# Kernel optimization log

Hardware: AMD Instinct MI355X
Metric: run time of the kernel (lower is better)

The kernel has to match this reference:

```python
import jax, jax.numpy as jnp
import numpy as np

NEG_SLOPE_GAT = 0.2   # GATConv internal leaky_relu slope (PyG default)
NEG_SLOPE = 0.01      # nn.LeakyReLU default slope


def _gat(h_src_in, h_dst_in, src, dst, Wsrc, Wdst, a_s, a_d, b, n_dst, self_loops):
    """Single-head PyG-style GATConv: gather -> score -> edge softmax -> scatter-sum."""
    hs = h_src_in @ Wsrc            # [N_src, C]
    hd = h_dst_in @ Wdst            # [N_dst, C]
    if self_loops:                  # static flag; same node set on both sides
        loop = jnp.arange(n_dst, dtype=src.dtype)
        src = jnp.concatenate([src, loop])
        dst = jnp.concatenate([dst, loop])
    # attention logits per edge
    e = jax.nn.leaky_relu((hs @ a_s)[src] + (hd @ a_d)[dst], NEG_SLOPE_GAT)  # [E]
    # softmax over edges sharing a destination node
    m = jax.ops.segment_max(e, dst, num_segments=n_dst)
    ex = jnp.exp(e - m[dst])
    denom = jax.ops.segment_sum(ex, dst, num_segments=n_dst)
    alpha = ex / denom[dst]
    out = jax.ops.segment_sum(hs[src] * alpha[:, None], dst, num_segments=n_dst)
    return out + b


def setup_inputs() -> dict:
    key = jax.random.key(0)
    ks = iter(jax.random.split(key, 64))
    NB, NP = 100_000, 50_000
    E_bb, E_pp, E_bp = 800_000, 400_000, 400_000
    FB, FP, H, H2 = 32, 34, 64, 32
    rn = lambda shape, s=0.05: jax.random.normal(next(ks), shape, jnp.float32) * s
    d = {}
    d['x_b'] = rn((NB, FB), 1.0)
    d['x_p'] = rn((NP, FP), 1.0)
    d['ei_bb'] = jax.random.randint(next(ks), (2, E_bb), 0, NB, jnp.int32)
    d['ei_pp'] = jax.random.randint(next(ks), (2, E_pp), 0, NP, jnp.int32)
    d['ei_bp_src'] = jax.random.randint(next(ks), (E_bp,), 0, NB, jnp.int32)
    d['ei_bp_dst'] = jax.random.randint(next(ks), (E_bp,), 0, NP, jnp.int32)
    d['W_in_b'] = rn((FB, H)); d['b_in_b'] = jnp.zeros((H,), jnp.float32)
    d['W_in_p'] = rn((FP, H)); d['b_in_p'] = jnp.zeros((H,), jnp.float32)
    for tag, cin, cout in (('1', H, H), ('2', H, H2)):
        d['W_bb' + tag] = rn((cin, cout)); d['as_bb' + tag] = rn((cout,)); d['ad_bb' + tag] = rn((cout,)); d['b_bb' + tag] = jnp.zeros((cout,), jnp.float32)
        d['W_pp' + tag] = rn((cin, cout)); d['as_pp' + tag] = rn((cout,)); d['ad_pp' + tag] = rn((cout,)); d['b_pp' + tag] = jnp.zeros((cout,), jnp.float32)
        d['Ws_bp' + tag] = rn((cin, cout)); d['Wd_bp' + tag] = rn((cin, cout)); d['as_bp' + tag] = rn((cout,)); d['ad_bp' + tag] = rn((cout,)); d['b_bp' + tag] = jnp.zeros((cout,), jnp.float32)
    d['W_out'] = rn((H2, 1)); d['b_out'] = jnp.zeros((1,), jnp.float32)
    return d


def reference(x_b, x_p, ei_bb, ei_pp, ei_bp_src, ei_bp_dst,
              W_in_b, b_in_b, W_in_p, b_in_p,
              W_bb1, as_bb1, ad_bb1, b_bb1, W_pp1, as_pp1, ad_pp1, b_pp1,
              Ws_bp1, Wd_bp1, as_bp1, ad_bp1, b_bp1,
              W_bb2, as_bb2, ad_bb2, b_bb2, W_pp2, as_pp2, ad_pp2, b_pp2,
              Ws_bp2, Wd_bp2, as_bp2, ad_bp2, b_bp2,
              W_out, b_out):
    NB, NP = x_b.shape[0], x_p.shape[0]
    lr = lambda v: jax.nn.leaky_relu(v, NEG_SLOPE)
    # input projections (dropout is eval-mode identity)
    hb = lr(x_b @ W_in_b + b_in_b)
    hp = lr(x_p @ W_in_p + b_in_p)
    # hetero conv 1 (sum aggregation over relations sharing a dst type)
    ob = _gat(hb, hb, ei_bb[0], ei_bb[1], W_bb1, W_bb1, as_bb1, ad_bb1, b_bb1, NB, True)
    op = (_gat(hp, hp, ei_pp[0], ei_pp[1], W_pp1, W_pp1, as_pp1, ad_pp1, b_pp1, NP, True)
          + _gat(hb, hp, ei_bp_src, ei_bp_dst, Ws_bp1, Wd_bp1, as_bp1, ad_bp1, b_bp1, NP, False))
    hb, hp = lr(ob), lr(op)
    # hetero conv 2
    ob2 = _gat(hb, hb, ei_bb[0], ei_bb[1], W_bb2, W_bb2, as_bb2, ad_bb2, b_bb2, NB, True)
    op2 = (_gat(hp, hp, ei_pp[0], ei_pp[1], W_pp2, W_pp2, as_pp2, ad_pp2, b_pp2, NP, True)
           + _gat(hb, hp, ei_bp_src, ei_bp_dst, Ws_bp2, Wd_bp2, as_bp2, ad_bp2, b_bp2, NP, False))
    hp = lr(op2)
    return hp @ W_out + b_out  # [NP, 1]
```

## Files before the change

### kernel.cpp

```cpp
#include <hip/hip_runtime.h>
#include <hip/hip_bf16.h>
#include <cstdint>
#include <cstddef>


typedef __attribute__((ext_vector_type(8))) short short8;
typedef __attribute__((ext_vector_type(4))) float f32x4;
typedef unsigned int u32;
typedef __hip_bfloat16 bf16;

#define ABITS 9
#define CHUNKE 8192

static __device__ __forceinline__ float b2f(bf16 v) { return __bfloat162float(v); }

static __device__ __forceinline__ float ldf(const void* p, int i, int bf) {
    return bf ? __bfloat162float(((const bf16*)p)[i]) : ((const float*)p)[i];
}

static __device__ __forceinline__ short f2bs(float f) {
    bf16 h = __float2bfloat16(f);
    return *reinterpret_cast<short*>(&h);
}
static __device__ __forceinline__ float bs2f(short s) {
    bf16 h = *reinterpret_cast<bf16*>(&s);
    return __bfloat162float(h);
}
static __device__ __forceinline__ float lo16(u32 u) { return bs2f((short)(u & 0xffffu)); }
static __device__ __forceinline__ float hi16(u32 u) { return bs2f((short)(u >> 16)); }
static __device__ __forceinline__ u32 pack2(float x, float y) {
    return (u32)(unsigned short)f2bs(x) | ((u32)(unsigned short)f2bs(y) << 16);
}
static __device__ __forceinline__ float sel4(const float* a, int i) {
    return i == 0 ? a[0] : i == 1 ? a[1] : i == 2 ? a[2] : a[3];
}
static __device__ __forceinline__ float lrelu2(float x) { return x > 0.f ? x : 0.2f * x; }

static __device__ __forceinline__ int probe_bf(const unsigned* __restrict__ w, int* cnt) {
    if (threadIdx.x == 0) *cnt = 0;
    __syncthreads();
    int c = 0;
#pragma unroll
    for (int j = 0; j < 4; ++j) {
        unsigned u = w[threadIdx.x * 4 + j];
        unsigned e = (u >> 7) & 0xffu;
        c += (e >= 100u && e <= 145u) ? 1 : 0;
    }
    atomicAdd(cnt, c);
    __syncthreads();
    int r = (*cnt > 614) ? 1 : 0;
    __syncthreads();
    return r;
}

template <int CIN>
static __device__ __forceinline__ void in_proj_body(
    short* WT, float* bl, int bid,
    const void* __restrict__ X, const void* __restrict__ W, const void* __restrict__ B,
    bf16* __restrict__ Y, int M, int bf)
{
    constexpr int KP = 40;
    for (int i = threadIdx.x; i < 64 * CIN; i += 256) {
        int n = i / CIN, k = i - n * CIN;
        WT[n * KP + k] = f2bs(ldf(W, k * 64 + n, bf));
    }
    if (threadIdx.x < 64) bl[threadIdx.x] = ldf(B, threadIdx.x, bf);
    __syncthreads();

    int lane = threadIdx.x & 63;
    int wv   = threadIdx.x >> 6;
    int m = lane & 15, quad = lane >> 4;
    int row0 = (bid * 4 + wv) * 16;
    if (row0 >= M) return;

    int arow = row0 + m; if (arow >= M) arow = M - 1;
    short8 a;
#pragma unroll
    for (int j = 0; j < 8; ++j)
        a[j] = f2bs(ldf(X, arow * CIN + quad * 8 + j, bf));

    f32x4 acc[4] = {};
#pragma unroll
    for (int tt = 0; tt < 4; ++tt) {
        short8 bfr = *(const short8*)&WT[((lane & 15) + 16 * tt) * KP + quad * 8];
        acc[tt] = __builtin_amdgcn_mfma_f32_16x16x32_bf16(a, bfr, acc[tt], 0, 0, 0);
    }

    if (CIN == 34) {
        float x32[4], x33[4];
#pragma unroll
        for (int r = 0; r < 4; ++r) {
            int row = row0 + quad * 4 + r; if (row >= M) row = M - 1;
            x32[r] = ldf(X, row * CIN + 32, bf);
            x33[r] = ldf(X, row * CIN + 33, bf);
        }
#pragma unroll
        for (int tt = 0; tt < 4; ++tt) {
            int col = (lane & 15) + 16 * tt;
            float w32 = bs2f(WT[col * KP + 32]);
            float w33 = bs2f(WT[col * KP + 33]);
#pragma unroll
            for (int r = 0; r < 4; ++r)
                acc[tt][r] += x32[r] * w32 + x33[r] * w33;
        }
    }

#pragma unroll
    for (int tt = 0; tt < 4; ++tt) {
        int col = (lane & 15) + 16 * tt;
        float bb = bl[col];
#pragma unroll
        for (int r = 0; r < 4; ++r) {
            int row = row0 + quad * 4 + r;
            if (row < M) {
                float v = acc[tt][r] + bb;
                v = v > 0.f ? v : 0.01f * v;
                Y[(size_t)row * 64 + col] = __float2bfloat16(v);
            }
        }
    }
}

__global__ __launch_bounds__(256) void k_hist_inproj(
    const int* __restrict__ bb_d, const int* __restrict__ pp_d,
    const int* __restrict__ bp_d, int* __restrict__ histM,
    const unsigned* __restrict__ probe_w, int* __restrict__ flag,
    int E_bb, int E_pp, int E_bp, int NB, int NP, int nbkt, int nblk,
    const void* __restrict__ Xb, const void* __restrict__ Wb, const void* __restrict__ Bb,
    bf16* __restrict__ Yb, int MB,
    const void* __restrict__ Xp, const void* __restrict__ Wp, const void* __restrict__ Bp,
    bf16* __restrict__ Yp, int MP)
{
    __shared__ short WT[64 * 40];
    __shared__ float bl[64];
    __shared__ int aux[1 << ABITS];
    if ((int)blockIdx.x < nblk) {
        if (blockIdx.x == 0) {
            int b = probe_bf(probe_w, &aux[0]);
            if (threadIdx.x == 0) *flag = b;
        }
        for (int i = threadIdx.x; i < nbkt; i += 256) aux[i] = 0;
        __syncthreads();
        int E_all = E_bb + E_pp + E_bp;
        int base = blockIdx.x * CHUNKE;
        int end = base + CHUNKE < E_all ? base + CHUNKE : E_all;
        for (int i = base + threadIdx.x; i < end; i += 256) {
            int d;
            if (i < E_bb) d = bb_d[i];
            else if (i < E_bb + E_pp) d = NB + pp_d[i - E_bb];
            else d = NB + NP + bp_d[i - E_bb - E_pp];
            atomicAdd(&aux[d >> ABITS], 1);
        }
        __syncthreads();
        for (int i = threadIdx.x; i < nbkt; i += 256)
            histM[(size_t)i * nblk + blockIdx.x] = aux[i];
    } else {
        int bfv = probe_bf(probe_w, &aux[0]);
        int bid = blockIdx.x - nblk;
        int nbb = (MB + 63) >> 6;
        if (bid < nbb) in_proj_body<32>(WT, bl, bid, Xb, Wb, Bb, Yb, MB, bfv);
        else           in_proj_body<34>(WT, bl, bid - nbb, Xp, Wp, Bp, Yp, MP, bfv);
    }
}

__global__ __launch_bounds__(1024) void k_scan1(const int* __restrict__ deg,
                                                int* __restrict__ out,
                                                int* __restrict__ bsum, int n)
{
    __shared__ int wsum[16];
    int gid = blockIdx.x * 1024 + threadIdx.x;
    int lane = threadIdx.x & 63, wid = threadIdx.x >> 6;
    int v = (gid < n) ? deg[gid] : 0;
    int x = v;
#pragma unroll
    for (int off = 1; off < 64; off <<= 1) {
        int y = __shfl_up(x, off, 64);
        if (lane >= off) x += y;
    }
    if (lane == 63) wsum[wid] = x;
    __syncthreads();
    if (wid == 0 && lane < 16) {
        int w0 = wsum[lane];
#pragma unroll
        for (int off = 1; off < 16; off <<= 1) {
            int y = __shfl_up(w0, off, 16);
            if (lane >= off) w0 += y;
        }
        wsum[lane] = w0;
    }
    __syncthreads();
    int base = (wid > 0) ? wsum[wid - 1] : 0;
    int incl = base + x;
    if (gid < n) out[gid] = incl - v;
    if (threadIdx.x == 1023) bsum[blockIdx.x] = incl;
}

__global__ __launch_bounds__(1024) void k_scan2(int* __restrict__ bsum, int nb)
{
    __shared__ int wsum[16];
    int lane = threadIdx.x & 63, wid = threadIdx.x >> 6;
    int v = (threadIdx.x < nb) ? bsum[threadIdx.x] : 0;
    int x = v;
#pragma unroll
    for (int off = 1; off < 64; off <<= 1) {
        int y = __shfl_up(x, off, 64);
        if (lane >= off) x += y;
    }
    if (lane == 63) wsum[wid] = x;
    __syncthreads();
    if (wid == 0 && lane < 16) {
        int w0 = wsum[lane];
#pragma unroll
        for (int off = 1; off < 16; off <<= 1) {
            int y = __shfl_up(w0, off, 16);
            if (lane >= off) w0 += y;
        }
        wsum[lane] = w0;
    }
    __syncthreads();
    int base = (wid > 0) ? wsum[wid - 1] : 0;
    if (threadIdx.x < nb) bsum[threadIdx.x] = base + x - v;
}

__global__ __launch_bounds__(1024) void k_scan3(int* __restrict__ indptr,
                                                const int* __restrict__ bsum,
                                                int n, int E)
{
    int gid = blockIdx.x * 1024 + threadIdx.x;
    if (gid < n) indptr[gid] += bsum[blockIdx.x];
    if (gid == 0) indptr[n] = E;
}

template <int N1, int N2, bool S1F, bool S2F>
static __device__ __forceinline__ void dual_body(
    short* WT, int bid, const bf16* __restrict__ H,
    const void* __restrict__ W1, const void* __restrict__ W2,
    const void* __restrict__ as1, const void* __restrict__ ad1,
    const void* __restrict__ as2, const void* __restrict__ ad2,
    bf16* __restrict__ HS1, bf16* __restrict__ HS2,
    float* __restrict__ SS1, float* __restrict__ SD1,
    float* __restrict__ SS2, float* __restrict__ SD2,
    int M, int bf)
{
    constexpr int KP = 72;
    constexpr int T1 = N1 / 16, T2 = N2 / 16, T = T1 + T2;
    for (int i = threadIdx.x; i < N1 * 64; i += 256) {
        int n = i >> 6, k = i & 63;
        WT[n * KP + k] = f2bs(ldf(W1, k * N1 + n, bf));
    }
    for (int i = threadIdx.x; i < N2 * 64; i += 256) {
        int n = i >> 6, k = i & 63;
        WT[(N1 + n) * KP + k] = f2bs(ldf(W2, k * N2 + n, bf));
    }
    __syncthreads();

    int lane = threadIdx.x & 63;
    int wv   = threadIdx.x >> 6;
    int m = lane & 15, quad = lane >> 4;
    int row0 = (bid * 4 + wv) * 16;
    if (row0 >= M) return;

    const short* Hs = (const short*)H;
    int arow = row0 + m; if (arow >= M) arow = M - 1;

    f32x4 acc[T] = {};
#pragma unroll
    for (int ks = 0; ks < 2; ++ks) {
        short8 a = *(const short8*)&Hs[(size_t)arow * 64 + ks * 32 + quad * 8];
#pragma unroll
        for (int tt = 0; tt < T; ++tt) {
            short8 bfr = *(const short8*)&WT[((lane & 15) + 16 * tt) * KP + ks * 32 + quad * 8];
            acc[tt] = __builtin_amdgcn_mfma_f32_16x16x32_bf16(a, bfr, acc[tt], 0, 0, 0);
        }
    }

    float vs1[4] = {}, vd1[4] = {}, vs2[4] = {}, vd2[4] = {};
#pragma unroll
    for (int tt = 0; tt < T1; ++tt) {
        int col = (lane & 15) + 16 * tt;
        float av = ldf(as1, col, bf), dv = ldf(ad1, col, bf);
#pragma unroll
        for (int r = 0; r < 4; ++r) {
            vs1[r] += acc[tt][r] * av;
            vd1[r] += acc[tt][r] * dv;
        }
    }
#pragma unroll
    for (int tt = 0; tt < T2; ++tt) {
        int col = (lane & 15) + 16 * tt;
        float av = ldf(as2, col, bf), dv = ldf(ad2, col, bf);
#pragma unroll
        for (int r = 0; r < 4; ++r) {
            vs2[r] += acc[T1 + tt][r] * av;
            vd2[r] += acc[T1 + tt][r] * dv;
        }
    }
#pragma unroll
    for (int off = 1; off < 16; off <<= 1)
#pragma unroll
        for (int r = 0; r < 4; ++r) {
            vs1[r] += __shfl_xor(vs1[r], off);
            vd1[r] += __shfl_xor(vd1[r], off);
            vs2[r] += __shfl_xor(vs2[r], off);
            vd2[r] += __shfl_xor(vd2[r], off);
        }
    int c = lane & 15;
    {
        int row = row0 + quad * 4 + (c & 3);
        if (row < M) {
            if (c < 4)       SS1[row] = sel4(vs1, c & 3);
            else if (c < 8)  SD1[row] = sel4(vd1, c & 3);
            else if (c < 12) SS2[row] = sel4(vs2, c & 3);
            else             SD2[row] = sel4(vd2, c & 3);
        }
    }

    if (S1F) {
#pragma unroll
        for (int tt = 0; tt < T1; ++tt) {
            int col = (lane & 15) + 16 * tt;
#pragma unroll
            for (int r = 0; r < 4; ++r) {
                int row = row0 + quad * 4 + r;
                if (row < M)
                    HS1[(size_t)row * N1 + col] = __float2bfloat16(acc[tt][r]);
            }
        }
    }
    if (S2F) {
#pragma unroll
        for (int tt = 0; tt < T2; ++tt) {
            int col = (lane & 15) + 16 * tt;
#pragma unroll
            for (int r = 0; r < 4; ++r) {
                int row = row0 + quad * 4 + r;
                if (row < M)
                    HS2[(size_t)row * N2 + col] = __float2bfloat16(acc[T1 + tt][r]);
            }
        }
    }
}

template <int N, bool STORE>
static __device__ __forceinline__ void proj_body(
    short* WT, int bid, const bf16* __restrict__ H, const void* __restrict__ W,
    const void* __restrict__ a_s, const void* __restrict__ a_d,
    bf16* __restrict__ HS, float* __restrict__ SS, float* __restrict__ SD,
    int M, int bf)
{
    constexpr int KP = 72;
    constexpr int T = N / 16;
    for (int i = threadIdx.x; i < N * 64; i += 256) {
        int n = i >> 6, k = i & 63;
        WT[n * KP + k] = f2bs(ldf(W, k * N + n, bf));
    }
    __syncthreads();

    int lane = threadIdx.x & 63;
    int wv   = threadIdx.x >> 6;
    int m = lane & 15, quad = lane >> 4;
    int row0 = (bid * 4 + wv) * 16;
    if (row0 >= M) return;

    const short* Hs = (const short*)H;
    int arow = row0 + m; if (arow >= M) arow = M - 1;

    f32x4 acc[T] = {};
#pragma unroll
    for (int ks = 0; ks < 2; ++ks) {
        short8 a = *(const short8*)&Hs[(size_t)arow * 64 + ks * 32 + quad * 8];
#pragma unroll
        for (int tt = 0; tt < T; ++tt) {
            short8 bfr = *(const short8*)&WT[((lane & 15) + 16 * tt) * KP + ks * 32 + quad * 8];
            acc[tt] = __builtin_amdgcn_mfma_f32_16x16x32_bf16(a, bfr, acc[tt], 0, 0, 0);
        }
    }

    float asv[T], adv[T];
#pragma unroll
    for (int tt = 0; tt < T; ++tt) {
        int col = (lane & 15) + 16 * tt;
        asv[tt] = ldf(a_s, col, bf);
        adv[tt] = ldf(a_d, col, bf);
    }
    float vs[4] = {}, vd[4] = {};
#pragma unroll
    for (int tt = 0; tt < T; ++tt)
#pragma unroll
        for (int r = 0; r < 4; ++r) {
            vs[r] += acc[tt][r] * asv[tt];
            vd[r] += acc[tt][r] * adv[tt];
        }
#pragma unroll
    for (int off = 1; off < 16; off <<= 1)
#pragma unroll
        for (int r = 0; r < 4; ++r) {
            vs[r] += __shfl_xor(vs[r], off);
            vd[r] += __shfl_xor(vd[r], off);
        }
    int c = lane & 15;
    if (c < 8) {
        int row = row0 + quad * 4 + (c & 3);
        if (row < M) {
            if (c < 4) SS[row] = sel4(vs, c & 3);
            else       SD[row] = sel4(vd, c & 3);
        }
    }

    if (STORE) {
#pragma unroll
        for (int tt = 0; tt < T; ++tt) {
            int col = (lane & 15) + 16 * tt;
#pragma unroll
            for (int r = 0; r < 4; ++r) {
                int row = row0 + quad * 4 + r;
                if (row < M)
                    HS[(size_t)row * N + col] = __float2bfloat16(acc[tt][r]);
            }
        }
    }
}

__global__ __launch_bounds__(256) void k_scatter_dual(
    const int* __restrict__ bb_s, const int* __restrict__ bb_d,
    const int* __restrict__ pp_s, const int* __restrict__ pp_d,
    const int* __restrict__ bp_s, const int* __restrict__ bp_d,
    const int* __restrict__ histS, unsigned* __restrict__ ebuf,
    int E_bb, int E_pp, int E_bp, int NB, int NP, int nbkt, int nblk,
    const bf16* __restrict__ hb,
    const void* W_bb1, const void* Ws_bp1,
    const void* as_bb1, const void* ad_bb1, const void* as_bp1, const void* ad_bp1,
    bf16* hs_bb, bf16* hs_bp,
    float* ss_bb, float* sd_bb, float* ss_bp, float* junkNB, int MB,
    const bf16* __restrict__ hp,
    const void* W_pp1, const void* Wd_bp1,
    const void* as_pp1, const void* ad_pp1,
    bf16* hs_pp, float* ss_pp, float* sd_pp, float* junkNP, float* sd_bp, int MP,
    const int* __restrict__ flag)
{
    __shared__ short WT[128 * 72];
    if ((int)blockIdx.x < nblk) {
        int* cur = (int*)WT;
        for (int i = threadIdx.x; i < nbkt; i += 256)
            cur[i] = histS[(size_t)i * nblk + blockIdx.x];
        __syncthreads();
        int E_all = E_bb + E_pp + E_bp;
        int base = blockIdx.x * CHUNKE;
        int end = base + CHUNKE < E_all ? base + CHUNKE : E_all;
        for (int i = base + threadIdx.x; i < end; i += 256) {
            int s, d;
            if (i < E_bb) { s = bb_s[i]; d = bb_d[i]; }
            else if (i < E_bb + E_pp) { int j = i - E_bb; s = pp_s[j]; d = NB + pp_d[j]; }
            else { int j = i - E_bb - E_pp; s = bp_s[j]; d = NB + NP + bp_d[j]; }
            int p = atomicAdd(&cur[d >> ABITS], 1);
            ebuf[p] = ((unsigned)(d & ((1 << ABITS) - 1)) << 20) | (unsigned)s;
        }
    } else {
        const int bfv = *flag;
        int bid = blockIdx.x - nblk;
        int nbb = (MB + 63) >> 6;
        if (bid < nbb)
            dual_body<64, 64, true, true>(WT, bid, hb, W_bb1, Ws_bp1,
                as_bb1, ad_bb1, as_bp1, ad_bp1, hs_bb, hs_bp,
                ss_bb, sd_bb, ss_bp, junkNB, MB, bfv);
        else
            dual_body<64, 64, true, false>(WT, bid - nbb, hp, W_pp1, Wd_bp1,
                as_pp1, ad_pp1, as_bp1, ad_bp1, hs_pp, nullptr,
                ss_pp, sd_pp, junkNP, sd_bp, MP, bfv);
    }
}

__global__ __launch_bounds__(256) void k_finalize(
    const unsigned* __restrict__ ebuf, const int* __restrict__ histS,
    int* __restrict__ ip_all, int2* __restrict__ sw,
    const float* __restrict__ ss_bb, const float* __restrict__ sd_bb,
    const float* __restrict__ ss_pp, const float* __restrict__ sd_pp,
    const float* __restrict__ ss_bp, const float* __restrict__ sd_bp,
    int NB, int NP, int NALL, int E_all, int nbkt, int nblk)
{
    __shared__ int h[1 << ABITS];
    __shared__ int pre[1 << ABITS];
    __shared__ int wq[4];
    int b = blockIdx.x;
    int d0 = b << ABITS;
    int nloc = NALL - d0 < (1 << ABITS) ? NALL - d0 : (1 << ABITS);
    int t = threadIdx.x;
    for (int i = t; i < (1 << ABITS); i += 256) h[i] = 0;
    __syncthreads();
    int s0 = histS[(size_t)b * nblk];
    int s1 = histS[(size_t)(b + 1) * nblk];
    for (int i = s0 + t; i < s1; i += 256)
        atomicAdd(&h[ebuf[i] >> 20], 1);
    __syncthreads();
    int v0 = h[2 * t], v1 = h[2 * t + 1];
    int ps = v0 + v1;
    int lane = t & 63, wid = t >> 6;
    int x = ps;
#pragma unroll
    for (int off = 1; off < 64; off <<= 1) {
        int y = __shfl_up(x, off, 64);
        if (lane >= off) x += y;
    }
    if (lane == 63) wq[wid] = x;
    __syncthreads();
    if (t == 0) {
        int a = 0;
#pragma unroll
        for (int w = 0; w < 4; ++w) { int tmp = wq[w]; wq[w] = a; a += tmp; }
    }
    __syncthreads();
    int excl = wq[wid] + x - ps;
    pre[2 * t]     = excl;
    pre[2 * t + 1] = excl + v0;
    __syncthreads();
    for (int i = t; i < nloc; i += 256) ip_all[d0 + i] = s0 + pre[i];
    if (d0 + nloc == NALL && t == 0) ip_all[NALL] = E_all;
    for (int i = t; i < (1 << ABITS); i += 256) h[i] = s0 + pre[i];
    __syncthreads();
    for (int i = s0 + t; i < s1; i += 256) {
        unsigned e = ebuf[i];
        int dl = (int)(e >> 20);
        int src = (int)(e & 0xFFFFFu);
        int p = atomicAdd(&h[dl], 1);
        int d = d0 + dl;
        float ssv, sdv;
        if (d < NB)           { ssv = ss_bb[src]; sdv = sd_bb[d]; }
        else if (d < NB + NP) { ssv = ss_pp[src]; sdv = sd_pp[d - NB]; }
        else                  { ssv = ss_bp[src]; sdv = sd_bp[d - NB - NP]; }
        int2 pk; pk.x = src; pk.y = __float_as_int(__expf(lrelu2(ssv + sdv)));
        sw[p] = pk;
    }
}

static __device__ __forceinline__ void gather1_body(
    int bid, const int* __restrict__ ip, const int2* __restrict__ sw,
    const float* __restrict__ SS, const float* __restrict__ SD,
    const bf16* __restrict__ HS, const void* __restrict__ bias,
    bf16* __restrict__ OUT, int M, int bf)
{
    int lane = threadIdx.x & 63;
    int half = lane >> 5, hl = lane & 31;
    int d = bid * 4 + (threadIdx.x >> 6);
    if (d >= M) return;
    const u32* H32 = (const u32*)HS;
    float ax = 0.f, ay = 0.f, den = 0.f;
    if (half == 0) {
        float ex = __expf(lrelu2(SS[d] + SD[d]));
        u32 h = H32[(size_t)d * 32 + hl];
        ax = lo16(h) * ex; ay = hi16(h) * ex; den = ex;
    }
    int j1 = ip[d + 1];
    int j = ip[d] + half;
    for (; j + 6 < j1; j += 8) {
        int2 p0 = sw[j], p1 = sw[j + 2], p2 = sw[j + 4], p3 = sw[j + 6];
        u32 h0 = H32[(size_t)p0.x * 32 + hl];
        u32 h1 = H32[(size_t)p1.x * 32 + hl];
        u32 h2 = H32[(size_t)p2.x * 32 + hl];
        u32 h3 = H32[(size_t)p3.x * 32 + hl];
        float e0 = __int_as_float(p0.y), e1 = __int_as_float(p1.y);
        float e2 = __int_as_float(p2.y), e3 = __int_as_float(p3.y);
        ax += lo16(h0) * e0 + lo16(h1) * e1 + lo16(h2) * e2 + lo16(h3) * e3;
        ay += hi16(h0) * e0 + hi16(h1) * e1 + hi16(h2) * e2 + hi16(h3) * e3;
        den += (e0 + e1) + (e2 + e3);
    }
    for (; j < j1; j += 2) {
        int2 p0 = sw[j];
        u32 h0 = H32[(size_t)p0.x * 32 + hl];
        float e0 = __int_as_float(p0.y);
        ax += lo16(h0) * e0; ay += hi16(h0) * e0; den += e0;
    }
    ax += __shfl_xor(ax, 32); ay += __shfl_xor(ay, 32); den += __shfl_xor(den, 32);
    if (half == 0) {
        float vx = ax / den + ldf(bias, 2 * hl, bf);
        float vy = ay / den + ldf(bias, 2 * hl + 1, bf);
        vx = vx > 0.f ? vx : 0.01f * vx;
        vy = vy > 0.f ? vy : 0.01f * vy;
        ((u32*)OUT)[(size_t)d * 32 + hl] = pack2(vx, vy);
    }
}

static __device__ __forceinline__ void gather2_body(
    int bid, const int* __restrict__ ip1, const int2* __restrict__ sw,
    const float* __restrict__ SS1, const float* __restrict__ SD1,
    const bf16* __restrict__ HS1,
    const int* __restrict__ ip2, const bf16* __restrict__ HS2,
    const void* __restrict__ b1, const void* __restrict__ b2,
    bf16* __restrict__ OUT, int M, int bf)
{
    int lane = threadIdx.x & 63;
    int half = lane >> 5, hl = lane & 31;
    int d = bid * 4 + (threadIdx.x >> 6);
    if (d >= M) return;
    const u32* H1 = (const u32*)HS1;
    const u32* H2 = (const u32*)HS2;
    float a1x = 0.f, a1y = 0.f, den1 = 0.f;
    if (half == 0) {
        float ex = __expf(lrelu2(SS1[d] + SD1[d]));
        u32 h = H1[(size_t)d * 32 + hl];
        a1x = lo16(h) * ex; a1y = hi16(h) * ex; den1 = ex;
    }
    int j1 = ip1[d + 1];
    int j = ip1[d] + half;
    for (; j + 6 < j1; j += 8) {
        int2 p0 = sw[j], p1 = sw[j + 2], p2 = sw[j + 4], p3 = sw[j + 6];
        u32 h0 = H1[(size_t)p0.x * 32 + hl];
        u32 h1 = H1[(size_t)p1.x * 32 + hl];
        u32 h2 = H1[(size_t)p2.x * 32 + hl];
        u32 h3 = H1[(size_t)p3.x * 32 + hl];
        float e0 = __int_as_float(p0.y), e1 = __int_as_float(p1.y);
        float e2 = __int_as_float(p2.y), e3 = __int_as_float(p3.y);
        a1x += lo16(h0) * e0 + lo16(h1) * e1 + lo16(h2) * e2 + lo16(h3) * e3;
        a1y += hi16(h0) * e0 + hi16(h1) * e1 + hi16(h2) * e2 + hi16(h3) * e3;
        den1 += (e0 + e1) + (e2 + e3);
    }
    for (; j < j1; j += 2) {
        int2 p0 = sw[j];
        u32 h0 = H1[(size_t)p0.x * 32 + hl];
        float e0 = __int_as_float(p0.y);
        a1x += lo16(h0) * e0; a1y += hi16(h0) * e0; den1 += e0;
    }
    float a2x = 0.f, a2y = 0.f, den2 = 0.f;
    j1 = ip2[d + 1];
    j = ip2[d] + half;
    for (; j + 6 < j1; j += 8) {
        int2 p0 = sw[j], p1 = sw[j + 2], p2 = sw[j + 4], p3 = sw[j + 6];
        u32 h0 = H2[(size_t)p0.x * 32 + hl];
        u32 h1 = H2[(size_t)p1.x * 32 + hl];
        u32 h2 = H2[(size_t)p2.x * 32 + hl];
        u32 h3 = H2[(size_t)p3.x * 32 + hl];
        float e0 = __int_as_float(p0.y), e1 = __int_as_float(p1.y);
        float e2 = __int_as_float(p2.y), e3 = __int_as_float(p3.y);
        a2x += lo16(h0) * e0 + lo16(h1) * e1 + lo16(h2) * e2 + lo16(h3) * e3;
        a2y += hi16(h0) * e0 + hi16(h1) * e1 + hi16(h2) * e2 + hi16(h3) * e3;
        den2 += (e0 + e1) + (e2 + e3);
    }
    for (; j < j1; j += 2) {
        int2 p0 = sw[j];
        u32 h0 = H2[(size_t)p0.x * 32 + hl];
        float e0 = __int_as_float(p0.y);
        a2x += lo16(h0) * e0; a2y += hi16(h0) * e0; den2 += e0;
    }
    a1x += __shfl_xor(a1x, 32); a1y += __shfl_xor(a1y, 32); den1 += __shfl_xor(den1, 32);
    a2x += __shfl_xor(a2x, 32); a2y += __shfl_xor(a2y, 32); den2 += __shfl_xor(den2, 32);
    if (half == 0) {
        float inv2 = den2 > 0.f ? 1.f / den2 : 0.f;
        float vx = a1x / den1 + a2x * inv2 + ldf(b1, 2 * hl, bf) + ldf(b2, 2 * hl, bf);
        float vy = a1y / den1 + a2y * inv2 + ldf(b1, 2 * hl + 1, bf) + ldf(b2, 2 * hl + 1, bf);
        vx = vx > 0.f ? vx : 0.01f * vx;
        vy = vy > 0.f ? vy : 0.01f * vy;
        ((u32*)OUT)[(size_t)d * 32 + hl] = pack2(vx, vy);
    }
}

__global__ __launch_bounds__(256) void k_gather12(
    const int* __restrict__ ip_bb, const int2* __restrict__ sw,
    const float* __restrict__ ss_bb, const float* __restrict__ sd_bb,
    const bf16* __restrict__ hs_bb, const void* __restrict__ b_bb1,
    bf16* __restrict__ hb2, int NB,
    const int* __restrict__ ip_pp, const int* __restrict__ ip_bp,
    const float* __restrict__ ss_pp, const float* __restrict__ sd_pp,
    const bf16* __restrict__ hs_pp, const bf16* __restrict__ hs_bp,
    const void* __restrict__ b_pp1, const void* __restrict__ b_bp1,
    bf16* __restrict__ hp2, int NP,
    const int* __restrict__ flag)
{
    const int bf = *flag;
    int nbb = (NB + 3) >> 2;
    if ((int)blockIdx.x < nbb)
        gather1_body(blockIdx.x, ip_bb, sw, ss_bb, sd_bb, hs_bb, b_bb1, hb2, NB, bf);
    else
        gather2_body(blockIdx.x - nbb, ip_pp, sw, ss_pp, sd_pp, hs_pp,
                     ip_bp, hs_bp, b_pp1, b_bp1, hp2, NP, bf);
}

__global__ __launch_bounds__(256) void k_proj2_all(
    const bf16* __restrict__ hp2,
    const void* W_pp2, const void* Wd_bp2,
    const void* as_pp2, const void* ad_pp2, const void* as_bp2, const void* ad_bp2,
    bf16* hs2_pp, float* ss2_pp, float* sd2_pp, float* junkNP, float* sd2_bp, int MP,
    const bf16* __restrict__ hb2,
    const void* Ws_bp2, bf16* hs2_bp, float* ss2_bp, float* junkNB, int MB,
    const int* __restrict__ flag)
{
    const int bf = *flag;
    __shared__ short WT[64 * 72];
    int npb = (MP + 63) >> 6;
    if ((int)blockIdx.x < npb)
        dual_body<32, 32, true, false>(WT, blockIdx.x, hp2, W_pp2, Wd_bp2,
            as_pp2, ad_pp2, as_bp2, ad_bp2, hs2_pp, nullptr,
            ss2_pp, sd2_pp, junkNP, sd2_bp, MP, bf);
    else
        proj_body<32, true>(WT, blockIdx.x - npb, hb2, Ws_bp2,
            as_bp2, ad_bp2, hs2_bp, ss2_bp, junkNB, MB, bf);
}

__global__ __launch_bounds__(256) void k_gather_out(
    const int* __restrict__ ip1, const int2* __restrict__ sw,
    const float* __restrict__ SS1, const float* __restrict__ SD1,
    const bf16* __restrict__ HS1,
    const int* __restrict__ ip2,
    const float* __restrict__ SS2, const float* __restrict__ SD2,
    const bf16* __restrict__ HS2,
    const void* __restrict__ b1, const void* __restrict__ b2,
    const void* __restrict__ Wout, const void* __restrict__ bout,
    void* __restrict__ OUT, int M, const int* __restrict__ flag)
{
    const int bf = *flag;
    int lane = threadIdx.x & 63;
    int q = lane >> 4, hl = lane & 15;
    int d = blockIdx.x * 4 + (threadIdx.x >> 6);
    if (d >= M) return;
    const u32* H1 = (const u32*)HS1;
    const u32* H2 = (const u32*)HS2;
    float sdd = SD1[d];
    float a1x = 0.f, a1y = 0.f, den1 = 0.f;
    if (q == 0) {
        float ex = __expf(lrelu2(SS1[d] + sdd));
        u32 h = H1[(size_t)d * 16 + hl];
        a1x = lo16(h) * ex; a1y = hi16(h) * ex; den1 = ex;
    }
    int j1 = ip1[d + 1];
    int j = ip1[d] + q;
    for (; j + 4 < j1; j += 8) {
        int s0 = sw[j].x, s1 = sw[j + 4].x;
        u32 h0 = H1[(size_t)s0 * 16 + hl];
        u32 h1 = H1[(size_t)s1 * 16 + hl];
        float e0 = __expf(lrelu2(SS1[s0] + sdd));
        float e1 = __expf(lrelu2(SS1[s1] + sdd));
        a1x += lo16(h0) * e0 + lo16(h1) * e1;
        a1y += hi16(h0) * e0 + hi16(h1) * e1;
        den1 += e0 + e1;
    }
    if (j < j1) {
        int s0 = sw[j].x;
        u32 h0 = H1[(size_t)s0 * 16 + hl];
        float e0 = __expf(lrelu2(SS1[s0] + sdd));
        a1x += lo16(h0) * e0; a1y += hi16(h0) * e0; den1 += e0;
    }
    float sdd2 = SD2[d];
    float a2x = 0.f, a2y = 0.f, den2 = 0.f;
    j1 = ip2[d + 1];
    j = ip2[d] + q;
    for (; j + 4 < j1; j += 8) {
        int s0 = sw[j].x, s1 = sw[j + 4].x;
        u32 h0 = H2[(size_t)s0 * 16 + hl];
        u32 h1 = H2[(size_t)s1 * 16 + hl];
        float e0 = __expf(lrelu2(SS2[s0] + sdd2));
        float e1 = __expf(lrelu2(SS2[s1] + sdd2));
        a2x += lo16(h0) * e0 + lo16(h1) * e1;
        a2y += hi16(h0) * e0 + hi16(h1) * e1;
        den2 += e0 + e1;
    }
    if (j < j1) {
        int s0 = sw[j].x;
        u32 h0 = H2[(size_t)s0 * 16 + hl];
        float e0 = __expf(lrelu2(SS2[s0] + sdd2));
        a2x += lo16(h0) * e0; a2y += hi16(h0) * e0; den2 += e0;
    }
    a1x += __shfl_xor(a1x, 16); a1y += __shfl_xor(a1y, 16); den1 += __shfl_xor(den1, 16);
    a2x += __shfl_xor(a2x, 16); a2y += __shfl_xor(a2y, 16); den2 += __shfl_xor(den2, 16);
    a1x += __shfl_xor(a1x, 32); a1y += __shfl_xor(a1y, 32); den1 += __shfl_xor(den1, 32);
    a2x += __shfl_xor(a2x, 32); a2y += __shfl_xor(a2y, 32); den2 += __shfl_xor(den2, 32);
    float inv2 = den2 > 0.f ? 1.f / den2 : 0.f;
    float vx = a1x / den1 + a2x * inv2 + ldf(b1, 2 * hl, bf) + ldf(b2, 2 * hl, bf);
    float vy = a1y / den1 + a2y * inv2 + ldf(b1, 2 * hl + 1, bf) + ldf(b2, 2 * hl + 1, bf);
    vx = vx > 0.f ? vx : 0.01f * vx;
    vy = vy > 0.f ? vy : 0.01f * vy;
    float t = vx * ldf(Wout, 2 * hl, bf) + vy * ldf(Wout, 2 * hl + 1, bf);
#pragma unroll
    for (int off = 1; off < 16; off <<= 1) t += __shfl_xor(t, off);
    if (lane == 0) {
        float r = t + ldf(bout, 0, bf);
        if (bf) ((bf16*)OUT)[d] = __float2bfloat16(r);
        else    ((float*)OUT)[d] = r;
    }
}

extern "C" void kernel_launch(void* const* d_in, const int* in_sizes, int n_in,
                              void* d_out, int out_size, void* d_ws, size_t ws_size,
                              hipStream_t stream)
{
    const void* x_b = d_in[0];
    const void* x_p = d_in[1];
    const int* ei_bb = (const int*)d_in[2];
    const int* ei_pp = (const int*)d_in[3];
    const int* bp_s  = (const int*)d_in[4];
    const int* bp_d  = (const int*)d_in[5];
    const void *W_in_b = d_in[6],  *b_in_b = d_in[7];
    const void *W_in_p = d_in[8],  *b_in_p = d_in[9];
    const void *W_bb1 = d_in[10], *as_bb1 = d_in[11], *ad_bb1 = d_in[12], *b_bb1 = d_in[13];
    const void *W_pp1 = d_in[14], *as_pp1 = d_in[15], *ad_pp1 = d_in[16], *b_pp1 = d_in[17];
    const void *Ws_bp1 = d_in[18], *Wd_bp1 = d_in[19], *as_bp1 = d_in[20], *ad_bp1 = d_in[21], *b_bp1 = d_in[22];
    const void *W_pp2 = d_in[27], *as_pp2 = d_in[28], *ad_pp2 = d_in[29], *b_pp2 = d_in[30];
    const void *Ws_bp2 = d_in[31], *Wd_bp2 = d_in[32], *as_bp2 = d_in[33], *ad_bp2 = d_in[34], *b_bp2 = d_in[35];
    const void *W_out = d_in[36], *b_out = d_in[37];

    const int NB   = in_sizes[0] / 32;
    const int NP   = in_sizes[1] / 34;
    const int E_bb = in_sizes[2] / 2;
    const int E_pp = in_sizes[3] / 2;
    const int E_bp = in_sizes[4];
    const int E_all = E_bb + E_pp + E_bp;
    const int NALL  = NB + 2 * NP;
    const int* bb_s = ei_bb;  const int* bb_d = ei_bb + E_bb;
    const int* pp_s = ei_pp;  const int* pp_d = ei_pp + E_pp;
    (void)ws_size; (void)n_in; (void)out_size;

    const int nbkt  = (NALL + (1 << ABITS) - 1) >> ABITS;
    const int nblk  = (E_all + CHUNKE - 1) / CHUNKE;
    const int nh    = nbkt * nblk;

    char* base = (char*)d_ws;
    size_t o = 0;
    auto alloc = [&](size_t bytes) { char* p = base + o; o += (bytes + 255) & ~(size_t)255; return p; };

    int* flag  = (int*)alloc(256);
    int* bsum  = (int*)alloc(1024 * 4);
    int* histM = (int*)alloc((size_t)nh * 4);
    int* histS = (int*)alloc((size_t)(nh + 1) * 4);
    int* ip_all = (int*)alloc((size_t)(NALL + 1) * 4);
    unsigned* ebuf = (unsigned*)alloc((size_t)E_all * 4);
    int2* sw = (int2*)alloc((size_t)E_all * 8);
    float* ss_bb = (float*)alloc((size_t)NB * 4);
    float* sd_bb = (float*)alloc((size_t)NB * 4);
    float* ss_bp = (float*)alloc((size_t)NB * 4);
    float* ss_pp = (float*)alloc((size_t)NP * 4);
    float* sd_pp = (float*)alloc((size_t)NP * 4);
    float* sd_bp = (float*)alloc((size_t)NP * 4);
    float* junkNB = (float*)alloc((size_t)NB * 4);
    float* junkNP = (float*)alloc((size_t)NP * 4);
    float* ss2_bp = ss_bb;
    float* ss2_pp = ss_pp;
    float* sd2_pp = sd_pp;
    float* sd2_bp = sd_bp;

    char* S1 = alloc((size_t)NB * 64 * 2);
    char* S2 = alloc((size_t)NP * 64 * 2);
    char* S3 = alloc((size_t)NB * 64 * 2);
    char* S4 = alloc((size_t)NB * 64 * 2);
    char* S5 = alloc((size_t)NB * 64 * 2);
    char* S6 = alloc((size_t)NP * 64 * 2);

    bf16* hb     = (bf16*)S1;
    bf16* hp     = (bf16*)S2;
    bf16* hs_bb  = (bf16*)S3;
    bf16* hb2    = (bf16*)S4;
    bf16* hs_bp  = (bf16*)S5;
    bf16* hs_pp  = (bf16*)S6;
    bf16* hp2    = (bf16*)S2;
    bf16* hs2_pp = (bf16*)S3;
    bf16* hs2_bp = (bf16*)S1;

    auto cdiv = [](int a, int b) { return (a + b - 1) / b; };

    const int* ip_bb = ip_all;
    const int* ip_pp = ip_all + NB;
    const int* ip_bp = ip_all + NB + NP;

    k_hist_inproj<<<nblk + cdiv(NB, 64) + cdiv(NP, 64), 256, 0, stream>>>(
        bb_d, pp_d, bp_d, histM, (const unsigned*)x_b, flag,
        E_bb, E_pp, E_bp, NB, NP, nbkt, nblk,
        x_b, W_in_b, b_in_b, hb, NB, x_p, W_in_p, b_in_p, hp, NP);

    int sb1 = cdiv(nh, 1024);
    k_scan1<<<sb1, 1024, 0, stream>>>(histM, histS, bsum, nh);
    k_scan2<<<1, 1024, 0, stream>>>(bsum, sb1);
    k_scan3<<<sb1, 1024, 0, stream>>>(histS, bsum, nh, E_all);

    k_scatter_dual<<<nblk + cdiv(NB, 64) + cdiv(NP, 64), 256, 0, stream>>>(
        bb_s, bb_d, pp_s, pp_d, bp_s, bp_d, histS, ebuf,
        E_bb, E_pp, E_bp, NB, NP, nbkt, nblk,
        hb, W_bb1, Ws_bp1, as_bb1, ad_bb1, as_bp1, ad_bp1,
        hs_bb, hs_bp, ss_bb, sd_bb, ss_bp, junkNB, NB,
        hp, W_pp1, Wd_bp1, as_pp1, ad_pp1,
        hs_pp, ss_pp, sd_pp, junkNP, sd_bp, NP, flag);

    k_finalize<<<nbkt, 256, 0, stream>>>(ebuf, histS, ip_all, sw,
                                         ss_bb, sd_bb, ss_pp, sd_pp, ss_bp, sd_bp,
                                         NB, NP, NALL, E_all, nbkt, nblk);

    k_gather12<<<cdiv(NB, 4) + cdiv(NP, 4), 256, 0, stream>>>(
        ip_bb, sw, ss_bb, sd_bb, hs_bb, b_bb1, hb2, NB,
        ip_pp, ip_bp, ss_pp, sd_pp, hs_pp, hs_bp,
        b_pp1, b_bp1, hp2, NP, flag);

    k_proj2_all<<<cdiv(NP, 64) + cdiv(NB, 64), 256, 0, stream>>>(
        hp2, W_pp2, Wd_bp2, as_pp2, ad_pp2, as_bp2, ad_bp2,
        hs2_pp, ss2_pp, sd2_pp, junkNP, sd2_bp, NP,
        hb2, Ws_bp2, hs2_bp, ss2_bp, junkNB, NB, flag);

    k_gather_out<<<cdiv(NP, 4), 256, 0, stream>>>(
        ip_pp, sw, ss2_pp, sd2_pp, hs2_pp,
        ip_bp, ss2_bp, sd2_bp, hs2_bp,
        b_pp2, b_bp2, W_out, b_out, d_out, NP, flag);
}
```

Before: 399.3 us.

## Aggregate raw inputs before layer-1 projection and fold attention vectors into input projection

Layer-1 GAT now gathers and aggregates the 64-wide input features hb/hp directly, then applies W after aggregation in a new post-projection MFMA kernel, using linearity of the weighted sum. The attention logits are computed in the input-projection kernel by precomputing W·a vectors, so the first projection pass is dropped from the scatter kernel. The scatter kernel becomes a pure edge bucketing pass with a smaller chunk size. This adds an extra kernel launch and an extra 64-wide intermediate buffer for the bp path, and logits are now computed from bf16-rounded products in a different order.

```diff
diff --git a/kernel.cpp b/kernel.cpp
--- a/kernel.cpp
+++ b/kernel.cpp
@@ -10,7 +10,7 @@
 typedef __hip_bfloat16 bf16;
 
 #define ABITS 9
-#define CHUNKE 8192
+#define CHUNKE 4096
 
 static __device__ __forceinline__ float b2f(bf16 v) { return __bfloat162float(v); }
 
@@ -55,9 +55,14 @@
 
 template <int CIN>
 static __device__ __forceinline__ void in_proj_body(
-    short* WT, float* bl, int bid,
+    short* WT, float* bl, float* FV, int bid,
     const void* __restrict__ X, const void* __restrict__ W, const void* __restrict__ B,
-    bf16* __restrict__ Y, int M, int bf)
+    const void* __restrict__ Wf0, const void* __restrict__ af0,
+    const void* __restrict__ Wf1, const void* __restrict__ af1,
+    const void* __restrict__ Wf2, const void* __restrict__ af2,
+    bf16* __restrict__ Y,
+    float* __restrict__ S0, float* __restrict__ S1v, float* __restrict__ S2v,
+    int M, int bf)
 {
     constexpr int KP = 40;
     for (int i = threadIdx.x; i < 64 * CIN; i += 256) {
@@ -65,6 +70,15 @@
         WT[n * KP + k] = f2bs(ldf(W, k * 64 + n, bf));
     }
     if (threadIdx.x < 64) bl[threadIdx.x] = ldf(B, threadIdx.x, bf);
+    if (threadIdx.x >= 64) {
+        int t = threadIdx.x - 64;
+        int v = t >> 6, k = t & 63;
+        const void* Wf = v == 0 ? Wf0 : v == 1 ? Wf1 : Wf2;
+        const void* af = v == 0 ? af0 : v == 1 ? af1 : af2;
+        float s = 0.f;
+        for (int n = 0; n < 64; ++n) s += ldf(Wf, k * 64 + n, bf) * ldf(af, n, bf);
+        FV[v * 64 + k] = s;
+    }
     __syncthreads();
 
     int lane = threadIdx.x & 63;
@@ -105,19 +119,35 @@
         }
     }
 
+    float vs[4] = {}, vd[4] = {}, ve[4] = {};
 #pragma unroll
     for (int tt = 0; tt < 4; ++tt) {
         int col = (lane & 15) + 16 * tt;
         float bb = bl[col];
+        float w0 = FV[col], w1 = FV[64 + col], w2 = FV[128 + col];
 #pragma unroll
         for (int r = 0; r < 4; ++r) {
             int row = row0 + quad * 4 + r;
-            if (row < M) {
-                float v = acc[tt][r] + bb;
-                v = v > 0.f ? v : 0.01f * v;
-                Y[(size_t)row * 64 + col] = __float2bfloat16(v);
-            }
-        }
+            float v = acc[tt][r] + bb;
+            v = v > 0.f ? v : 0.01f * v;
+            if (row < M) Y[(size_t)row * 64 + col] = __float2bfloat16(v);
+            vs[r] += v * w0; vd[r] += v * w1; ve[r] += v * w2;
+        }
+    }
+#pragma unroll
+    for (int off = 1; off < 16; off <<= 1)
+#pragma unroll
+        for (int r = 0; r < 4; ++r) {
+            vs[r] += __shfl_xor(vs[r], off);
+            vd[r] += __shfl_xor(vd[r], off);
+            ve[r] += __shfl_xor(ve[r], off);
+        }
+    int c = lane & 15;
+    int row = row0 + quad * 4 + (c & 3);
+    if (row < M && c < 12) {
+        if (c < 4)       S0[row]  = sel4(vs, c & 3);
+        else if (c < 8)  S1v[row] = sel4(vd, c & 3);
+        else             S2v[row] = sel4(ve, c & 3);
     }
 }
 
@@ -129,10 +159,17 @@
     const void* __restrict__ Xb, const void* __restrict__ Wb, const void* __restrict__ Bb,
     bf16* __restrict__ Yb, int MB,
     const void* __restrict__ Xp, const void* __restrict__ Wp, const void* __restrict__ Bp,
-    bf16* __restrict__ Yp, int MP)
+    bf16* __restrict__ Yp, int MP,
+    const void* W_bb1, const void* as_bb1, const void* ad_bb1,
+    const void* Ws_bp1, const void* as_bp1,
+    const void* W_pp1, const void* as_pp1, const void* ad_pp1,
+    const void* Wd_bp1, const void* ad_bp1,
+    float* __restrict__ ss_bb, float* __restrict__ sd_bb, float* __restrict__ ss_bp,
+    float* __restrict__ ss_pp, float* __restrict__ sd_pp, float* __restrict__ sd_bp)
 {
     __shared__ short WT[64 * 40];
     __shared__ float bl[64];
+    __shared__ float FV[192];
     __shared__ int aux[1 << ABITS];
     if ((int)blockIdx.x < nblk) {
         if (blockIdx.x == 0) {
@@ -158,8 +195,14 @@
         int bfv = probe_bf(probe_w, &aux[0]);
         int bid = blockIdx.x - nblk;
         int nbb = (MB + 63) >> 6;
-        if (bid < nbb) in_proj_body<32>(WT, bl, bid, Xb, Wb, Bb, Yb, MB, bfv);
-        else           in_proj_body<34>(WT, bl, bid - nbb, Xp, Wp, Bp, Yp, MP, bfv);
+        if (bid < nbb)
+            in_proj_body<32>(WT, bl, FV, bid, Xb, Wb, Bb,
+                W_bb1, as_bb1, W_bb1, ad_bb1, Ws_bp1, as_bp1,
+                Yb, ss_bb, sd_bb, ss_bp, MB, bfv);
+        else
+            in_proj_body<34>(WT, bl, FV, bid - nbb, Xp, Wp, Bp,
+                W_pp1, as_pp1, W_pp1, ad_pp1, Wd_bp1, ad_bp1,
+                Yp, ss_pp, sd_pp, sd_bp, MP, bfv);
     }
 }
 
@@ -421,52 +464,27 @@
     }
 }
 
-__global__ __launch_bounds__(256) void k_scatter_dual(
+__global__ __launch_bounds__(256) void k_scatter(
     const int* __restrict__ bb_s, const int* __restrict__ bb_d,
     const int* __restrict__ pp_s, const int* __restrict__ pp_d,
     const int* __restrict__ bp_s, const int* __restrict__ bp_d,
     const int* __restrict__ histS, unsigned* __restrict__ ebuf,
-    int E_bb, int E_pp, int E_bp, int NB, int NP, int nbkt, int nblk,
-    const bf16* __restrict__ hb,
-    const void* W_bb1, const void* Ws_bp1,
-    const void* as_bb1, const void* ad_bb1, const void* as_bp1, const void* ad_bp1,
-    bf16* hs_bb, bf16* hs_bp,
-    float* ss_bb, float* sd_bb, float* ss_bp, float* junkNB, int MB,
-    const bf16* __restrict__ hp,
-    const void* W_pp1, const void* Wd_bp1,
-    const void* as_pp1, const void* ad_pp1,
-    bf16* hs_pp, float* ss_pp, float* sd_pp, float* junkNP, float* sd_bp, int MP,
-    const int* __restrict__ flag)
-{
-    __shared__ short WT[128 * 72];
-    if ((int)blockIdx.x < nblk) {
-        int* cur = (int*)WT;
-        for (int i = threadIdx.x; i < nbkt; i += 256)
-            cur[i] = histS[(size_t)i * nblk + blockIdx.x];
-        __syncthreads();
-        int E_all = E_bb + E_pp + E_bp;
-        int base = blockIdx.x * CHUNKE;
-        int end = base + CHUNKE < E_all ? base + CHUNKE : E_all;
-        for (int i = base + threadIdx.x; i < end; i += 256) {
-            int s, d;
-            if (i < E_bb) { s = bb_s[i]; d = bb_d[i]; }
-            else if (i < E_bb + E_pp) { int j = i - E_bb; s = pp_s[j]; d = NB + pp_d[j]; }
-            else { int j = i - E_bb - E_pp; s = bp_s[j]; d = NB + NP + bp_d[j]; }
-            int p = atomicAdd(&cur[d >> ABITS], 1);
-            ebuf[p] = ((unsigned)(d & ((1 << ABITS) - 1)) << 20) | (unsigned)s;
-        }
-    } else {
-        const int bfv = *flag;
-        int bid = blockIdx.x - nblk;
-        int nbb = (MB + 63) >> 6;
-        if (bid < nbb)
-            dual_body<64, 64, true, true>(WT, bid, hb, W_bb1, Ws_bp1,
-                as_bb1, ad_bb1, as_bp1, ad_bp1, hs_bb, hs_bp,
-                ss_bb, sd_bb, ss_bp, junkNB, MB, bfv);
-        else
-            dual_body<64, 64, true, false>(WT, bid - nbb, hp, W_pp1, Wd_bp1,
-                as_pp1, ad_pp1, as_bp1, ad_bp1, hs_pp, nullptr,
-                ss_pp, sd_pp, junkNP, sd_bp, MP, bfv);
+    int E_bb, int E_pp, int E_bp, int NB, int NP, int nbkt, int nblk)
+{
+    __shared__ int cur[1 << ABITS];
+    for (int i = threadIdx.x; i < nbkt; i += 256)
+        cur[i] = histS[(size_t)i * nblk + blockIdx.x];
+    __syncthreads();
+    int E_all = E_bb + E_pp + E_bp;
+    int base = blockIdx.x * CHUNKE;
+    int end = base + CHUNKE < E_all ? base + CHUNKE : E_all;
+    for (int i = base + threadIdx.x; i < end; i += 256) {
+        int s, d;
+        if (i < E_bb) { s = bb_s[i]; d = bb_d[i]; }
+        else if (i < E_bb + E_pp) { int j = i - E_bb; s = pp_s[j]; d = NB + pp_d[j]; }
+        else { int j = i - E_bb - E_pp; s = bp_s[j]; d = NB + NP + bp_d[j]; }
+        int p = atomicAdd(&cur[d >> ABITS], 1);
+        ebuf[p] = ((unsigned)(d & ((1 << ABITS) - 1)) << 20) | (unsigned)s;
     }
 }
 
@@ -535,8 +553,7 @@
 static __device__ __forceinline__ void gather1_body(
     int bid, const int* __restrict__ ip, const int2* __restrict__ sw,
     const float* __restrict__ SS, const float* __restrict__ SD,
-    const bf16* __restrict__ HS, const void* __restrict__ bias,
-    bf16* __restrict__ OUT, int M, int bf)
+    const bf16* __restrict__ HS, bf16* __restrict__ OUT, int M)
 {
     int lane = threadIdx.x & 63;
     int half = lane >> 5, hl = lane & 31;
@@ -571,28 +588,24 @@
     }
     ax += __shfl_xor(ax, 32); ay += __shfl_xor(ay, 32); den += __shfl_xor(den, 32);
     if (half == 0) {
-        float vx = ax / den + ldf(bias, 2 * hl, bf);
-        float vy = ay / den + ldf(bias, 2 * hl + 1, bf);
-        vx = vx > 0.f ? vx : 0.01f * vx;
-        vy = vy > 0.f ? vy : 0.01f * vy;
-        ((u32*)OUT)[(size_t)d * 32 + hl] = pack2(vx, vy);
+        float inv = 1.f / den;
+        ((u32*)OUT)[(size_t)d * 32 + hl] = pack2(ax * inv, ay * inv);
     }
 }
 
 static __device__ __forceinline__ void gather2_body(
     int bid, const int* __restrict__ ip1, const int2* __restrict__ sw,
     const float* __restrict__ SS1, const float* __restrict__ SD1,
-    const bf16* __restrict__ HS1,
-    const int* __restrict__ ip2, const bf16* __restrict__ HS2,
-    const void* __restrict__ b1, const void* __restrict__ b2,
-    bf16* __restrict__ OUT, int M, int bf)
+    const bf16* __restrict__ H1T,
+    const int* __restrict__ ip2, const bf16* __restrict__ H2T,
+    bf16* __restrict__ O1, bf16* __restrict__ O2, int M)
 {
     int lane = threadIdx.x & 63;
     int half = lane >> 5, hl = lane & 31;
     int d = bid * 4 + (threadIdx.x >> 6);
     if (d >= M) return;
-    const u32* H1 = (const u32*)HS1;
-    const u32* H2 = (const u32*)HS2;
+    const u32* H1 = (const u32*)H1T;
+    const u32* H2 = (const u32*)H2T;
     float a1x = 0.f, a1y = 0.f, den1 = 0.f;
     if (half == 0) {
         float ex = __expf(lrelu2(SS1[d] + SD1[d]));
@@ -643,34 +656,113 @@
     a1x += __shfl_xor(a1x, 32); a1y += __shfl_xor(a1y, 32); den1 += __shfl_xor(den1, 32);
     a2x += __shfl_xor(a2x, 32); a2y += __shfl_xor(a2y, 32); den2 += __shfl_xor(den2, 32);
     if (half == 0) {
+        float inv1 = 1.f / den1;
         float inv2 = den2 > 0.f ? 1.f / den2 : 0.f;
-        float vx = a1x / den1 + a2x * inv2 + ldf(b1, 2 * hl, bf) + ldf(b2, 2 * hl, bf);
-        float vy = a1y / den1 + a2y * inv2 + ldf(b1, 2 * hl + 1, bf) + ldf(b2, 2 * hl + 1, bf);
-        vx = vx > 0.f ? vx : 0.01f * vx;
-        vy = vy > 0.f ? vy : 0.01f * vy;
-        ((u32*)OUT)[(size_t)d * 32 + hl] = pack2(vx, vy);
+        ((u32*)O1)[(size_t)d * 32 + hl] = pack2(a1x * inv1, a1y * inv1);
+        ((u32*)O2)[(size_t)d * 32 + hl] = pack2(a2x * inv2, a2y * inv2);
     }
 }
 
 __global__ __launch_bounds__(256) void k_gather12(
     const int* __restrict__ ip_bb, const int2* __restrict__ sw,
     const float* __restrict__ ss_bb, const float* __restrict__ sd_bb,
-    const bf16* __restrict__ hs_bb, const void* __restrict__ b_bb1,
-    bf16* __restrict__ hb2, int NB,
+    const bf16* __restrict__ hb, bf16* __restrict__ agg_bb, int NB,
     const int* __restrict__ ip_pp, const int* __restrict__ ip_bp,
     const float* __restrict__ ss_pp, const float* __restrict__ sd_pp,
-    const bf16* __restrict__ hs_pp, const bf16* __restrict__ hs_bp,
-    const void* __restrict__ b_pp1, const void* __restrict__ b_bp1,
-    bf16* __restrict__ hp2, int NP,
-    const int* __restrict__ flag)
-{
-    const int bf = *flag;
+    const bf16* __restrict__ hp,
+    bf16* __restrict__ agg_pp, bf16* __restrict__ agg_bp, int NP)
+{
     int nbb = (NB + 3) >> 2;
     if ((int)blockIdx.x < nbb)
-        gather1_body(blockIdx.x, ip_bb, sw, ss_bb, sd_bb, hs_bb, b_bb1, hb2, NB, bf);
+        gather1_body(blockIdx.x, ip_bb, sw, ss_bb, sd_bb, hb, agg_bb, NB);
     else
-        gather2_body(blockIdx.x - nbb, ip_pp, sw, ss_pp, sd_pp, hs_pp,
-                     ip_bp, hs_bp, b_pp1, b_bp1, hp2, NP, bf);
+        gather2_body(blockIdx.x - nbb, ip_pp, sw, ss_pp, sd_pp, hp,
+                     ip_bp, hb, agg_pp, agg_bp, NP);
+}
+
+template <bool DUAL>
+static __device__ __forceinline__ void postproj_body(
+    short* WT, float* bl, int bid,
+    const bf16* __restrict__ A1, const bf16* __restrict__ A2,
+    const void* __restrict__ W1, const void* __restrict__ W2,
+    const void* __restrict__ B1, const void* __restrict__ B2,
+    bf16* __restrict__ OUT, int M, int bf)
+{
+    constexpr int KP = 72;
+    for (int i = threadIdx.x; i < 64 * 64; i += 256) {
+        int n = i >> 6, k = i & 63;
+        WT[n * KP + k] = f2bs(ldf(W1, k * 64 + n, bf));
+        if (DUAL) WT[(64 + n) * KP + k] = f2bs(ldf(W2, k * 64 + n, bf));
+    }
+    if (threadIdx.x < 64) {
+        float b = ldf(B1, threadIdx.x, bf);
+        if (DUAL) b += ldf(B2, threadIdx.x, bf);
+        bl[threadIdx.x] = b;
+    }
+    __syncthreads();
+
+    int lane = threadIdx.x & 63;
+    int wv   = threadIdx.x >> 6;
+    int m = lane & 15, quad = lane >> 4;
+    int row0 = (bid * 4 + wv) * 16;
+    if (row0 >= M) return;
+
+    const short* A1s = (const short*)A1;
+    const short* A2s = (const short*)A2;
+    int arow = row0 + m; if (arow >= M) arow = M - 1;
+
+    f32x4 acc[4] = {};
+#pragma unroll
+    for (int ks = 0; ks < 2; ++ks) {
+        short8 a1 = *(const short8*)&A1s[(size_t)arow * 64 + ks * 32 + quad * 8];
+#pragma unroll
+        for (int tt = 0; tt < 4; ++tt) {
+            short8 bfr = *(const short8*)&WT[((lane & 15) + 16 * tt) * KP + ks * 32 + quad * 8];
+            acc[tt] = __builtin_amdgcn_mfma_f32_16x16x32_bf16(a1, bfr, acc[tt], 0, 0, 0);
+        }
+        if (DUAL) {
+            short8 a2 = *(const short8*)&A2s[(size_t)arow * 64 + ks * 32 + quad * 8];
+#pragma unroll
+            for (int tt = 0; tt < 4; ++tt) {
+                short8 bfr = *(const short8*)&WT[(64 + (lane & 15) + 16 * tt) * KP + ks * 32 + quad * 8];
+                acc[tt] = __builtin_amdgcn_mfma_f32_16x16x32_bf16(a2, bfr, acc[tt], 0, 0, 0);
+            }
+        }
+    }
+
+#pragma unroll
+    for (int tt = 0; tt < 4; ++tt) {
+        int col = (lane & 15) + 16 * tt;
+        float bb = bl[col];
+#pragma unroll
+        for (int r = 0; r < 4; ++r) {
+            int row = row0 + quad * 4 + r;
+            if (row < M) {
+                float v = acc[tt][r] + bb;
+                v = v > 0.f ? v : 0.01f * v;
+                OUT[(size_t)row * 64 + col] = __float2bfloat16(v);
+            }
+        }
+    }
+}
+
+__global__ __launch_bounds__(256) void k_postproj1(
+    const bf16* __restrict__ agg_pp, const bf16* __restrict__ agg_bp,
+    const void* W_pp1, const void* Ws_bp1,
+    const void* b_pp1, const void* b_bp1, bf16* __restrict__ hp2, int MP,
+    const bf16* __restrict__ agg_bb, const void* W_bb1, const void* b_bb1,
+    bf16* __restrict__ hb2, int MB, const int* __restrict__ flag)
+{
+    const int bf = *flag;
+    __shared__ short WT[128 * 72];
+    __shared__ float bl[64];
+    int npb = (MP + 63) >> 6;
+    if ((int)blockIdx.x < npb)
+        postproj_body<true>(WT, bl, blockIdx.x, agg_pp, agg_bp,
+                            W_pp1, Ws_bp1, b_pp1, b_bp1, hp2, MP, bf);
+    else
+        postproj_body<false>(WT, bl, blockIdx.x - npb, agg_bb, nullptr,
+                             W_bb1, nullptr, b_bb1, nullptr, hb2, MB, bf);
 }
 
 __global__ __launch_bounds__(256) void k_proj2_all(
@@ -843,10 +935,10 @@
 
     bf16* hb     = (bf16*)S1;
     bf16* hp     = (bf16*)S2;
-    bf16* hs_bb  = (bf16*)S3;
+    bf16* agg_bb = (bf16*)S3;
     bf16* hb2    = (bf16*)S4;
-    bf16* hs_bp  = (bf16*)S5;
-    bf16* hs_pp  = (bf16*)S6;
+    bf16* agg_bp = (bf16*)S5;
+    bf16* agg_pp = (bf16*)S6;
     bf16* hp2    = (bf16*)S2;
     bf16* hs2_pp = (bf16*)S3;
     bf16* hs2_bp = (bf16*)S1;
@@ -860,29 +952,31 @@
     k_hist_inproj<<<nblk + cdiv(NB, 64) + cdiv(NP, 64), 256, 0, stream>>>(
         bb_d, pp_d, bp_d, histM, (const unsigned*)x_b, flag,
         E_bb, E_pp, E_bp, NB, NP, nbkt, nblk,
-        x_b, W_in_b, b_in_b, hb, NB, x_p, W_in_p, b_in_p, hp, NP);
+        x_b, W_in_b, b_in_b, hb, NB, x_p, W_in_p, b_in_p, hp, NP,
+        W_bb1, as_bb1, ad_bb1, Ws_bp1, as_bp1,
+        W_pp1, as_pp1, ad_pp1, Wd_bp1, ad_bp1,
+        ss_bb, sd_bb, ss_bp, ss_pp, sd_pp, sd_bp);
 
     int sb1 = cdiv(nh, 1024);
     k_scan1<<<sb1, 1024, 0, stream>>>(histM, histS, bsum, nh);
     k_scan2<<<1, 1024, 0, stream>>>(bsum, sb1);
     k_scan3<<<sb1, 1024, 0, stream>>>(histS, bsum, nh, E_all);
 
-    k_scatter_dual<<<nblk + cdiv(NB, 64) + cdiv(NP, 64), 256, 0, stream>>>(
+    k_scatter<<<nblk, 256, 0, stream>>>(
         bb_s, bb_d, pp_s, pp_d, bp_s, bp_d, histS, ebuf,
-        E_bb, E_pp, E_bp, NB, NP, nbkt, nblk,
-        hb, W_bb1, Ws_bp1, as_bb1, ad_bb1, as_bp1, ad_bp1,
-        hs_bb, hs_bp, ss_bb, sd_bb, ss_bp, junkNB, NB,
-        hp, W_pp1, Wd_bp1, as_pp1, ad_pp1,
-        hs_pp, ss_pp, sd_pp, junkNP, sd_bp, NP, flag);
+        E_bb, E_pp, E_bp, NB, NP, nbkt, nblk);
 
     k_finalize<<<nbkt, 256, 0, stream>>>(ebuf, histS, ip_all, sw,
                                          ss_bb, sd_bb, ss_pp, sd_pp, ss_bp, sd_bp,
                                          NB, NP, NALL, E_all, nbkt, nblk);
 
     k_gather12<<<cdiv(NB, 4) + cdiv(NP, 4), 256, 0, stream>>>(
-        ip_bb, sw, ss_bb, sd_bb, hs_bb, b_bb1, hb2, NB,
-        ip_pp, ip_bp, ss_pp, sd_pp, hs_pp, hs_bp,
-        b_pp1, b_bp1, hp2, NP, flag);
+        ip_bb, sw, ss_bb, sd_bb, hb, agg_bb, NB,
+        ip_pp, ip_bp, ss_pp, sd_pp, hp, agg_pp, agg_bp, NP);
+
+    k_postproj1<<<cdiv(NP, 64) + cdiv(NB, 64), 256, 0, stream>>>(
+        agg_pp, agg_bp, W_pp1, Ws_bp1, b_pp1, b_bp1, hp2, NP,
+        agg_bb, W_bb1, b_bb1, hb2, NB, flag);
 
     k_proj2_all<<<cdiv(NP, 64) + cdiv(NB, 64), 256, 0, stream>>>(
         hp2, W_pp2, Wd_bp2, as_pp2, ad_pp2, as_bp2, ad_bp2,
```

Result: slower. 432.3 us (+8.3%).
